# Kernel optimization log

Hardware: AMD Instinct MI355X
Metric: run time of the kernel (lower is better)

The kernel has to match this reference:

```python
import jax, jax.numpy as jnp
import numpy as np

ALPHA = 0.2       # LeakyReLU negative slope
ADJ_THRE = 0.0
NEG_INF = -1e30   # finite stand-in for -inf (safe in fp32 softmax)


def setup_inputs() -> dict:
    key = jax.random.key(0)
    k1, k2, k3, k4, k5, k6 = jax.random.split(key, 6)
    b, n_k = 4, 512
    in_f, e_in_f, out_f = 256, 64, 256
    x = jax.random.normal(k1, (b, n_k, in_f), dtype=jnp.float32)
    edge = jax.random.normal(k2, (b, n_k, n_k, e_in_f), dtype=jnp.float32)
    adj = jax.random.uniform(k3, (b, n_k, n_k), dtype=jnp.float32)
    # xavier_uniform with gain=1.414
    def xavier(k, shape, gain=1.414):
        fan_in, fan_out = shape[0], shape[1]
        bound = gain * np.sqrt(6.0 / (fan_in + fan_out))
        return jax.random.uniform(k, shape, dtype=jnp.float32, minval=-bound, maxval=bound)
    W = xavier(k4, (in_f, out_f))
    W1 = xavier(k5, (e_in_f, out_f))
    a = xavier(k6, (3 * out_f, 1))
    return {"x": x, "edge": edge, "adj": adj, "W": W, "W1": W1, "a": a}


def reference(x, edge, adj, W, W1, a):
    # x:(b,n,in_f) edge:(b,n,n,e_in) adj:(b,n,n)
    out_f = W.shape[1]
    h = jnp.matmul(x, W)                      # (b, n, o)
    a1 = a[:out_f, 0]                         # score weight for h_i (row)
    a2 = a[out_f:2 * out_f, 0]                # score weight for h_j (col)
    a3 = a[2 * out_f:, 0]                     # score weight for edge proj
    # concat([h_i, h_j, e_h]) @ a == h_i@a1 + h_j@a2 + (edge@W1)@a3
    s_i = jnp.einsum('bno,o->bn', h, a1)      # (b, n)
    s_j = jnp.einsum('bno,o->bn', h, a2)      # (b, n)
    w1a3 = W1 @ a3                            # (e_in,) fused: edge@(W1@a3)
    s_e = jnp.einsum('bije,e->bij', edge, w1a3)  # (b, n, n)
    e = jax.nn.leaky_relu(s_i[:, :, None] + s_j[:, None, :] + s_e, ALPHA)
    e = jnp.where(adj > ADJ_THRE, e, NEG_INF)
    attention = jax.nn.softmax(e, axis=2)     # (b, n, n); dropout off (eval)
    h_prime = jnp.matmul(attention, h)        # (b, n, o)
    return jax.nn.elu(h_prime)                # concat=True
```

## Files before the change

kernel.cpp:

```cpp
#include <hip/hip_runtime.h>
#include <cstdint>
#include <cstddef>

#define ALPHA 0.2f
#define NEG_INF -1e30f

constexpr int B = 4, N = 512, IN_F = 256, E_F = 64, OUT_F = 256;

__global__ __launch_bounds__(256) void k_h(const float* __restrict__ x,
                                           const float* __restrict__ W,
                                           const float* __restrict__ W1,
                                           const float* __restrict__ a,
                                           float* __restrict__ h,
                                           float* __restrict__ s_i,
                                           float* __restrict__ s_j,
                                           float* __restrict__ w1a3) {
    int tid = threadIdx.x;
    if (blockIdx.x == (B * N) / 4) {
        int e = tid >> 2, part = tid & 3;
        const float* row = W1 + (size_t)e * OUT_F + part * 64;
        const float* a3 = a + 2 * OUT_F + part * 64;
        float s = 0.f;
        #pragma unroll 8
        for (int o = 0; o < 64; ++o) s += row[o] * a3[o];
        s += __shfl_xor(s, 1);
        s += __shfl_xor(s, 2);
        if (part == 0) w1a3[e] = s;
        return;
    }
    int wv = tid >> 6, lane = tid & 63;
    int row = blockIdx.x * 4 + wv;
    int c4 = lane * 4;

    __shared__ float xs[4][IN_F];
    *(float4*)&xs[wv][c4] = *(const float4*)&x[(size_t)row * IN_F + c4];
    __syncthreads();

    float4 acc = {0.f, 0.f, 0.f, 0.f};
    for (int k = 0; k < IN_F; ++k) {
        float4 w4 = *(const float4*)&W[(size_t)k * OUT_F + c4];
        float xv = xs[wv][k];
        acc.x = fmaf(xv, w4.x, acc.x);
        acc.y = fmaf(xv, w4.y, acc.y);
        acc.z = fmaf(xv, w4.z, acc.z);
        acc.w = fmaf(xv, w4.w, acc.w);
    }
    *(float4*)&h[(size_t)row * OUT_F + c4] = acc;

    float4 a1v = *(const float4*)&a[c4];
    float4 a2v = *(const float4*)&a[OUT_F + c4];
    float p1 = acc.x * a1v.x + acc.y * a1v.y + acc.z * a1v.z + acc.w * a1v.w;
    float p2 = acc.x * a2v.x + acc.y * a2v.y + acc.z * a2v.z + acc.w * a2v.w;
    #pragma unroll
    for (int off = 32; off; off >>= 1) {
        p1 += __shfl_xor(p1, off);
        p2 += __shfl_xor(p2, off);
    }
    if (lane == 0) { s_i[row] = p1; s_j[row] = p2; }
}

__global__ __launch_bounds__(256) void k_att(const float* __restrict__ edge,
                                             const float* __restrict__ adj,
                                             const float* __restrict__ s_i,
                                             const float* __restrict__ s_j,
                                             const float* __restrict__ w1a3,
                                             float* __restrict__ att) {
    int bi = blockIdx.x;
    int b = bi >> 9;
    int tid = threadIdx.x;
    int wv = tid >> 6, lane = tid & 63;
    int jl = lane >> 2;
    int p = lane & 3;

    __shared__ float w1a3s[E_F];
    __shared__ float sjs[N];
    __shared__ float adjs[N];
    __shared__ float part[N][4];
    __shared__ float redm[4], reds[4];

    if (tid < E_F) w1a3s[tid] = w1a3[tid];
    sjs[tid]        = s_j[b * N + tid];
    sjs[tid + 256]  = s_j[b * N + tid + 256];
    adjs[tid]       = adj[(size_t)bi * N + tid];
    adjs[tid + 256] = adj[(size_t)bi * N + tid + 256];
    float si = s_i[bi];
    __syncthreads();

    float4 wa = *(const float4*)&w1a3s[p * 16];
    float4 wb = *(const float4*)&w1a3s[p * 16 + 4];
    float4 wc = *(const float4*)&w1a3s[p * 16 + 8];
    float4 wd = *(const float4*)&w1a3s[p * 16 + 12];

    const float* ebase = edge + (size_t)bi * N * E_F;
    for (int it = 0; it < 8; ++it) {
        int j = it * 64 + wv * 16 + jl;
        const float4* ej = (const float4*)(ebase + (size_t)j * E_F + p * 16);
        float4 e0 = ej[0];
        float4 e1 = ej[1];
        float4 e2 = ej[2];
        float4 e3 = ej[3];
        float s = e0.x * wa.x + e0.y * wa.y + e0.z * wa.z + e0.w * wa.w;
        s = fmaf(e1.x, wb.x, s); s = fmaf(e1.y, wb.y, s);
        s = fmaf(e1.z, wb.z, s); s = fmaf(e1.w, wb.w, s);
        s = fmaf(e2.x, wc.x, s); s = fmaf(e2.y, wc.y, s);
        s = fmaf(e2.z, wc.z, s); s = fmaf(e2.w, wc.w, s);
        s = fmaf(e3.x, wd.x, s); s = fmaf(e3.y, wd.y, s);
        s = fmaf(e3.z, wd.z, s); s = fmaf(e3.w, wd.w, s);
        part[j][p] = s;
    }
    __syncthreads();

    float v0 = si + sjs[tid] + part[tid][0] + part[tid][1] + part[tid][2] + part[tid][3];
    float v1 = si + sjs[tid + 256] + part[tid + 256][0] + part[tid + 256][1]
             + part[tid + 256][2] + part[tid + 256][3];
    v0 = v0 > 0.f ? v0 : ALPHA * v0;
    v1 = v1 > 0.f ? v1 : ALPHA * v1;
    v0 = (adjs[tid] > 0.f) ? v0 : NEG_INF;
    v1 = (adjs[tid + 256] > 0.f) ? v1 : NEG_INF;

    float m = fmaxf(v0, v1);
    #pragma unroll
    for (int off = 32; off; off >>= 1) m = fmaxf(m, __shfl_xor(m, off));
    if (lane == 0) redm[wv] = m;
    __syncthreads();
    m = fmaxf(fmaxf(redm[0], redm[1]), fmaxf(redm[2], redm[3]));

    float e0 = __expf(v0 - m);
    float e1 = __expf(v1 - m);
    float s = e0 + e1;
    #pragma unroll
    for (int off = 32; off; off >>= 1) s += __shfl_xor(s, off);
    if (lane == 0) reds[wv] = s;
    __syncthreads();
    s = reds[0] + reds[1] + reds[2] + reds[3];
    float inv = 1.f / s;

    att[(size_t)bi * N + tid]       = e0 * inv;
    att[(size_t)bi * N + tid + 256] = e1 * inv;
}

__global__ __launch_bounds__(256) void k_out(const float* __restrict__ att,
                                             const float* __restrict__ h,
                                             float* __restrict__ out) {
    int row0 = blockIdx.x * 4;
    int b = row0 >> 9;
    int tid = threadIdx.x;
    int wv = tid >> 6, lane = tid & 63;

    __shared__ float as_[4][N];
    {
        const float* arow = att + (size_t)(row0 + wv) * N + lane * 8;
        *(float4*)&as_[wv][lane * 8]     = *(const float4*)arow;
        *(float4*)&as_[wv][lane * 8 + 4] = *(const float4*)(arow + 4);
    }
    __syncthreads();

    int c4 = lane * 4;
    const float* hb = h + (size_t)b * N * OUT_F;
    float4 acc = {0.f, 0.f, 0.f, 0.f};
    for (int k = 0; k < N; ++k) {
        float4 hv = *(const float4*)&hb[(size_t)k * OUT_F + c4];
        float av = as_[wv][k];
        acc.x = fmaf(av, hv.x, acc.x);
        acc.y = fmaf(av, hv.y, acc.y);
        acc.z = fmaf(av, hv.z, acc.z);
        acc.w = fmaf(av, hv.w, acc.w);
    }
    float4 o4;
    o4.x = acc.x > 0.f ? acc.x : (expf(acc.x) - 1.f);
    o4.y = acc.y > 0.f ? acc.y : (expf(acc.y) - 1.f);
    o4.z = acc.z > 0.f ? acc.z : (expf(acc.z) - 1.f);
    o4.w = acc.w > 0.f ? acc.w : (expf(acc.w) - 1.f);
    *(float4*)&out[(size_t)(row0 + wv) * OUT_F + c4] = o4;
}

extern "C" void kernel_launch(void* const* d_in, const int* in_sizes, int n_in,
                              void* d_out, int out_size, void* d_ws, size_t ws_size,
                              hipStream_t stream) {
    const float* x    = (const float*)d_in[0];
    const float* edge = (const float*)d_in[1];
    const float* adj  = (const float*)d_in[2];
    const float* W    = (const float*)d_in[3];
    const float* W1   = (const float*)d_in[4];
    const float* a    = (const float*)d_in[5];
    float* out = (float*)d_out;

    float* ws = (float*)d_ws;
    float* h_buf    = ws;
    float* att_buf  = h_buf + (size_t)B * N * OUT_F;
    float* si_buf   = att_buf + (size_t)B * N * N;
    float* sj_buf   = si_buf + B * N;
    float* w1a3_buf = sj_buf + B * N;

    k_h<<<(B * N) / 4 + 1, 256, 0, stream>>>(x, W, W1, a, h_buf, si_buf, sj_buf, w1a3_buf);
    k_att<<<B * N, 256, 0, stream>>>(edge, adj, si_buf, sj_buf, w1a3_buf, att_buf);
    k_out<<<(B * N) / 4, 256, 0, stream>>>(att_buf, h_buf, out);
}
```

Measured before the change: 467.5 us.

## Fuse attention softmax with attention-times-h aggregation and coalesce edge loads

Merges the attention kernel and the output matmul kernel so each block computes one softmax row, keeps it in shared memory, and immediately multiplies it by h with a split-K across four waves and a shared-memory reduction. This removes the global write and re-read of the full attention matrix and one kernel launch. The edge-score loop is also restructured so 16 consecutive lanes read one contiguous 256-byte edge row as float4s into a padded 17-wide partial buffer, giving fully coalesced loads. The trade-off is that each block now streams 512x256 of h per output row instead of sharing it across four rows, which raises L2 traffic for h, and shared memory usage grows.

After: 409.5 us. 12.4% less time.

```diff
diff --git a/kernel.cpp b/kernel.cpp
--- a/kernel.cpp
+++ b/kernel.cpp
@@ -59,23 +59,22 @@
     if (lane == 0) { s_i[row] = p1; s_j[row] = p2; }
 }
 
-__global__ __launch_bounds__(256) void k_att(const float* __restrict__ edge,
-                                             const float* __restrict__ adj,
-                                             const float* __restrict__ s_i,
-                                             const float* __restrict__ s_j,
-                                             const float* __restrict__ w1a3,
-                                             float* __restrict__ att) {
+__global__ __launch_bounds__(256) void k_att_out(const float* __restrict__ edge,
+                                                 const float* __restrict__ adj,
+                                                 const float* __restrict__ s_i,
+                                                 const float* __restrict__ s_j,
+                                                 const float* __restrict__ w1a3,
+                                                 const float* __restrict__ h,
+                                                 float* __restrict__ out) {
     int bi = blockIdx.x;
     int b = bi >> 9;
     int tid = threadIdx.x;
     int wv = tid >> 6, lane = tid & 63;
-    int jl = lane >> 2;
-    int p = lane & 3;
 
-    __shared__ float w1a3s[E_F];
+    __shared__ __align__(16) float part[N][17];
     __shared__ float sjs[N];
     __shared__ float adjs[N];
-    __shared__ float part[N][4];
+    __shared__ __align__(16) float w1a3s[E_F];
     __shared__ float redm[4], reds[4];
 
     if (tid < E_F) w1a3s[tid] = w1a3[tid];
@@ -86,33 +85,30 @@
     float si = s_i[bi];
     __syncthreads();
 
-    float4 wa = *(const float4*)&w1a3s[p * 16];
-    float4 wb = *(const float4*)&w1a3s[p * 16 + 4];
-    float4 wc = *(const float4*)&w1a3s[p * 16 + 8];
-    float4 wd = *(const float4*)&w1a3s[p * 16 + 12];
+    int col = lane & 15;
+    int jg  = lane >> 4;
+    float4 w4 = *(const float4*)&w1a3s[col * 4];
+    const float* ebase = edge + (size_t)bi * N * E_F;
 
-    const float* ebase = edge + (size_t)bi * N * E_F;
+    #pragma unroll
     for (int it = 0; it < 8; ++it) {
-        int j = it * 64 + wv * 16 + jl;
-        const float4* ej = (const float4*)(ebase + (size_t)j * E_F + p * 16);
-        float4 e0 = ej[0];
-        float4 e1 = ej[1];
-        float4 e2 = ej[2];
-        float4 e3 = ej[3];
-        float s = e0.x * wa.x + e0.y * wa.y + e0.z * wa.z + e0.w * wa.w;
-        s = fmaf(e1.x, wb.x, s); s = fmaf(e1.y, wb.y, s);
-        s = fmaf(e1.z, wb.z, s); s = fmaf(e1.w, wb.w, s);
-        s = fmaf(e2.x, wc.x, s); s = fmaf(e2.y, wc.y, s);
-        s = fmaf(e2.z, wc.z, s); s = fmaf(e2.w, wc.w, s);
-        s = fmaf(e3.x, wd.x, s); s = fmaf(e3.y, wd.y, s);
-        s = fmaf(e3.z, wd.z, s); s = fmaf(e3.w, wd.w, s);
-        part[j][p] = s;
+        int jw = it * 64 + wv * 16;
+        #pragma unroll
+        for (int i = 0; i < 4; ++i) {
+            int j = jw + i * 4 + jg;
+            float4 ev = *(const float4*)(ebase + (size_t)j * E_F + col * 4);
+            part[j][col] = ev.x * w4.x + ev.y * w4.y + ev.z * w4.z + ev.w * w4.w;
+        }
     }
     __syncthreads();
 
-    float v0 = si + sjs[tid] + part[tid][0] + part[tid][1] + part[tid][2] + part[tid][3];
-    float v1 = si + sjs[tid + 256] + part[tid + 256][0] + part[tid + 256][1]
-             + part[tid + 256][2] + part[tid + 256][3];
+    float v0 = si + sjs[tid];
+    float v1 = si + sjs[tid + 256];
+    #pragma unroll
+    for (int c = 0; c < 16; ++c) {
+        v0 += part[tid][c];
+        v1 += part[tid + 256][c];
+    }
     v0 = v0 > 0.f ? v0 : ALPHA * v0;
     v1 = v1 > 0.f ? v1 : ALPHA * v1;
     v0 = (adjs[tid] > 0.f) ? v0 : NEG_INF;
@@ -135,43 +131,27 @@
     s = reds[0] + reds[1] + reds[2] + reds[3];
     float inv = 1.f / s;
 
-    att[(size_t)bi * N + tid]       = e0 * inv;
-    att[(size_t)bi * N + tid + 256] = e1 * inv;
-}
-
-__global__ __launch_bounds__(256) void k_out(const float* __restrict__ att,
-                                             const float* __restrict__ h,
-                                             float* __restrict__ out) {
-    int row0 = blockIdx.x * 4;
-    int b = row0 >> 9;
-    int tid = threadIdx.x;
-    int wv = tid >> 6, lane = tid & 63;
-
-    __shared__ float as_[4][N];
-    {
-        const float* arow = att + (size_t)(row0 + wv) * N + lane * 8;
-        *(float4*)&as_[wv][lane * 8]     = *(const float4*)arow;
-        *(float4*)&as_[wv][lane * 8 + 4] = *(const float4*)(arow + 4);
-    }
+    sjs[tid]       = e0 * inv;
+    sjs[tid + 256] = e1 * inv;
     __syncthreads();
 
+    const float* hb = h + (size_t)b * N * OUT_F;
     int c4 = lane * 4;
-    const float* hb = h + (size_t)b * N * OUT_F;
     float4 acc = {0.f, 0.f, 0.f, 0.f};
-    for (int k = 0; k < N; ++k) {
+    int k0 = wv * 128;
+    for (int k = k0; k < k0 + 128; ++k) {
+        float av = sjs[k];
         float4 hv = *(const float4*)&hb[(size_t)k * OUT_F + c4];
-        float av = as_[wv][k];
         acc.x = fmaf(av, hv.x, acc.x);
         acc.y = fmaf(av, hv.y, acc.y);
         acc.z = fmaf(av, hv.z, acc.z);
         acc.w = fmaf(av, hv.w, acc.w);
     }
-    float4 o4;
-    o4.x = acc.x > 0.f ? acc.x : (expf(acc.x) - 1.f);
-    o4.y = acc.y > 0.f ? acc.y : (expf(acc.y) - 1.f);
-    o4.z = acc.z > 0.f ? acc.z : (expf(acc.z) - 1.f);
-    o4.w = acc.w > 0.f ? acc.w : (expf(acc.w) - 1.f);
-    *(float4*)&out[(size_t)(row0 + wv) * OUT_F + c4] = o4;
+    float* flat = &part[0][0];
+    ((float4*)(flat + wv * 256))[lane] = acc;
+    __syncthreads();
+    float r = flat[tid] + flat[256 + tid] + flat[512 + tid] + flat[768 + tid];
+    out[(size_t)bi * OUT_F + tid] = r > 0.f ? r : (expf(r) - 1.f);
 }
 
 extern "C" void kernel_launch(void* const* d_in, const int* in_sizes, int n_in,
@@ -187,12 +167,10 @@
 
     float* ws = (float*)d_ws;
     float* h_buf    = ws;
-    float* att_buf  = h_buf + (size_t)B * N * OUT_F;
-    float* si_buf   = att_buf + (size_t)B * N * N;
+    float* si_buf   = h_buf + (size_t)B * N * OUT_F;
     float* sj_buf   = si_buf + B * N;
     float* w1a3_buf = sj_buf + B * N;
 
     k_h<<<(B * N) / 4 + 1, 256, 0, stream>>>(x, W, W1, a, h_buf, si_buf, sj_buf, w1a3_buf);
-    k_att<<<B * N, 256, 0, stream>>>(edge, adj, si_buf, sj_buf, w1a3_buf, att_buf);
-    k_out<<<(B * N) / 4, 256, 0, stream>>>(att_buf, h_buf, out);
+    k_att_out<<<B * N, 256, 0, stream>>>(edge, adj, si_buf, sj_buf, w1a3_buf, h_buf, out);
 }
```
